# Kernel optimization log

Hardware: AMD Instinct MI355X
Metric: run time of the kernel (lower is better)

Reference implementation:

```python
import jax, jax.numpy as jnp
import numpy as np

N_Q = 8  # number of residual quantization levels


def setup_inputs() -> dict:
    key = jax.random.key(0)
    k1, k2 = jax.random.split(key)
    hidden_states = jax.random.normal(k1, (8192, 128), dtype=jnp.float32)
    codebooks = jax.random.normal(k2, (N_Q, 256, 128), dtype=jnp.float32)
    return {"hidden_states": hidden_states, "codebooks": codebooks}


def reference(hidden_states, codebooks):
    """Residual VQ encode: per level, nearest codebook entry by L2, subtract, accumulate.

    hidden_states: [N, D]; codebooks: [n_q, bins, D].
    Returns (codes [n_q, N] int, quantized [N, D]).
    """
    residual = hidden_states
    quantized = jnp.zeros_like(hidden_states)
    codes = []
    for i in range(N_Q):  # small fixed loop over structurally distinct levels
        codebook = codebooks[i]  # [bins, D]
        # squared L2 distance, same math as the original broadcasted form
        dist = jnp.sum((residual[:, None, :] - codebook[None, :, :]) ** 2, axis=-1)  # [N, bins]
        idx = jnp.argmin(dist, axis=-1)  # [N]
        chosen = codebook[idx]  # [N, D]
        quantized = quantized + chosen
        residual = residual - chosen
        codes.append(idx)
    return jnp.stack(codes, axis=0), quantized
```

## Files before the change

### kernel.cpp

```cpp
#include <hip/hip_runtime.h>

#define NQ 8
#define BINS 256
#define D 128
#define RPB 16
#define THREADS 512
#define RSTRIDE 132
#define FREG 520

typedef short s8v __attribute__((ext_vector_type(8)));
typedef short s4v __attribute__((ext_vector_type(4)));
typedef float f4v __attribute__((ext_vector_type(4)));

static __device__ __forceinline__ unsigned short bf16_rtne(float x) {
    unsigned u = __float_as_uint(x);
    unsigned r = (u + 0x7fffu + ((u >> 16) & 1u)) >> 16;
    return (unsigned short)r;
}
static __device__ __forceinline__ float bf16_to_f(unsigned short h) {
    return __uint_as_float(((unsigned)h) << 16);
}
struct Split3 { short h, m, l; };
static __device__ __forceinline__ Split3 split3(float x) {
    Split3 s;
    unsigned short hb = bf16_rtne(x);
    float r1 = x - bf16_to_f(hb);
    unsigned short mb = bf16_rtne(r1);
    unsigned short lb = bf16_rtne(r1 - bf16_to_f(mb));
    s.h = (short)hb; s.m = (short)mb; s.l = (short)lb;
    return s;
}
static __device__ __forceinline__ unsigned long long u64min(unsigned long long a, unsigned long long b) {
    return a < b ? a : b;
}
static __device__ __forceinline__ unsigned long long shfl_xor_u64(unsigned long long v, int mask) {
    int lo = (int)(unsigned)(v & 0xffffffffull);
    int hi = (int)(unsigned)(v >> 32);
    lo = __shfl_xor(lo, mask, 64);
    hi = __shfl_xor(hi, mask, 64);
    return ((unsigned long long)(unsigned)hi << 32) | (unsigned)lo;
}

__global__ __launch_bounds__(256) void rvq_prep(
    const float* __restrict__ cb, short* __restrict__ cb_hi,
    short* __restrict__ cb_mid, short* __restrict__ cb_lo,
    float* __restrict__ c2)
{
    __shared__ float st[16 * RSTRIDE];
    const int L = blockIdx.x >> 4;
    const int o = blockIdx.x & 15;
    const int t = threadIdx.x;

    const float4* src = (const float4*)(cb + ((size_t)L * BINS + o * 16) * D);
    #pragma unroll
    for (int i = 0; i < 2; ++i) {
        int f4 = i * 256 + t;
        int row = f4 >> 5, c4 = f4 & 31;
        float4 v = src[f4];
        float* d = &st[row * RSTRIDE + c4 * 4];
        d[0] = v.x; d[1] = v.y; d[2] = v.z; d[3] = v.w;
    }
    __syncthreads();

    const int bin = t >> 4;
    const int kc  = t & 15;
    const float* p = &st[bin * RSTRIDE + kc * 8];
    s8v h8, m8, l8;
    float s = 0.f;
    #pragma unroll
    for (int j = 0; j < 8; ++j) {
        float x = p[j];
        Split3 sp = split3(x);
        h8[j] = sp.h; m8[j] = sp.m; l8[j] = sp.l;
        s = fmaf(x, x, s);
    }
    int idx = (L * 16 + kc) * BINS + (o * 16 + bin);
    ((s8v*)cb_hi)[idx]  = h8;
    ((s8v*)cb_mid)[idx] = m8;
    ((s8v*)cb_lo)[idx]  = l8;
    s += __shfl_xor(s, 1, 64);
    s += __shfl_xor(s, 2, 64);
    s += __shfl_xor(s, 4, 64);
    s += __shfl_xor(s, 8, 64);
    if (kc == 0) c2[L * BINS + o * 16 + bin] = s;
}

static __device__ __forceinline__ void frag_store4(
    const float* rres, short* ah, short* am, short* al, int rr_, int g8, int half)
{
    s4v h4, m4, l4;
    #pragma unroll
    for (int j = 0; j < 4; ++j) {
        Split3 sp = split3(rres[j]);
        h4[j] = sp.h; m4[j] = sp.m; l4[j] = sp.l;
    }
    int q  = g8 & 3;
    int ks = g8 >> 2;
    int idx16 = q * 16 + ((rr_ + 4 * q) & 15);
    int off = ks * FREG + idx16 * 8 + half * 4;
    *(s4v*)&ah[off] = h4;
    *(s4v*)&am[off] = m4;
    *(s4v*)&al[off] = l4;
}

static __device__ __forceinline__ void issue_cb(
    int lv, int base16, int m, int quad,
    const s8v* __restrict__ bhp, const s8v* __restrict__ bmp, const s8v* __restrict__ blp,
    const float* __restrict__ c2p,
    s8v bh[4], s8v bm[4], s8v bl[4], f4v& c2v)
{
    const int bin = base16 + m;
    #pragma unroll
    for (int ks = 0; ks < 4; ++ks) {
        int idx = (lv * 16 + ks * 4 + quad) * BINS + bin;
        bh[ks] = bhp[idx];
        bm[ks] = bmp[idx];
        bl[ks] = blp[idx];
    }
    c2v = *(const f4v*)(c2p + lv * BINS + base16 + quad * 4);
}

static __device__ __forceinline__ unsigned long long cluster(
    const s8v bh[4], const s8v bm[4], const s8v bl[4],
    const s8v rfh[4], const s8v rfm[4], const s8v rfl[4],
    f4v c2c, int binbase, unsigned long long best)
{
    f4v a0 = {0.f, 0.f, 0.f, 0.f};
    f4v a1 = {0.f, 0.f, 0.f, 0.f};
    f4v a2 = {0.f, 0.f, 0.f, 0.f};
    __builtin_amdgcn_s_setprio(1);
    #pragma unroll
    for (int ks = 0; ks < 4; ++ks) {
        a0 = __builtin_amdgcn_mfma_f32_16x16x32_bf16(bh[ks], rfh[ks], a0, 0, 0, 0);
        a1 = __builtin_amdgcn_mfma_f32_16x16x32_bf16(bm[ks], rfh[ks], a1, 0, 0, 0);
        a1 = __builtin_amdgcn_mfma_f32_16x16x32_bf16(bh[ks], rfm[ks], a1, 0, 0, 0);
        a2 = __builtin_amdgcn_mfma_f32_16x16x32_bf16(bm[ks], rfm[ks], a2, 0, 0, 0);
        a2 = __builtin_amdgcn_mfma_f32_16x16x32_bf16(bl[ks], rfh[ks], a2, 0, 0, 0);
        a2 = __builtin_amdgcn_mfma_f32_16x16x32_bf16(bh[ks], rfl[ks], a2, 0, 0, 0);
    }
    __builtin_amdgcn_s_setprio(0);
    #pragma unroll
    for (int i = 0; i < 4; ++i) {
        float dot = a0[i] + (a1[i] + a2[i]);
        float k = fmaf(-2.f, dot, c2c[i]);
        unsigned u = __float_as_uint(k);
        u = (u & 0x80000000u) ? ~u : (u | 0x80000000u);
        best = u64min(best, ((unsigned long long)u << 32) | (unsigned)(binbase + i));
    }
    return best;
}

__global__ __launch_bounds__(THREADS)
__attribute__((amdgpu_waves_per_eu(2, 4)))
void rvq_kernel(
    const float* __restrict__ hidden,
    const float* __restrict__ cb_f32,
    const short* __restrict__ cb_hi,
    const short* __restrict__ cb_mid,
    const short* __restrict__ cb_lo,
    const float* __restrict__ c2p,
    float* __restrict__ out_codes,
    float* __restrict__ out_quant,
    int N)
{
    __shared__ __align__(16) short ah[4 * FREG];
    __shared__ __align__(16) short am[4 * FREG];
    __shared__ __align__(16) short al[4 * FREG];
    __shared__ __align__(16) unsigned long long redw[RPB][10];

    const int t = threadIdx.x;
    const int w = t >> 6;
    const int l = t & 63;
    const int quad = l >> 4;
    const int m = l & 15;
    const int woff = w * 32;
    const int row0 = blockIdx.x * RPB;
    const int rr_  = t >> 5;
    const int gd   = t & 31;
    const int g8   = gd >> 1;
    const int half = gd & 1;
    const int dbase = g8 * 8 + half * 4;

    float rres[4], hreg[4];
    {
        const f4v* hp = (const f4v*)(hidden + (size_t)(row0 + rr_) * D + dbase);
        f4v v = *hp;
        #pragma unroll
        for (int j = 0; j < 4; ++j) { hreg[j] = v[j]; rres[j] = v[j]; }
    }
    frag_store4(rres, ah, am, al, rr_, g8, half);

    const s8v* bhp = (const s8v*)cb_hi;
    const s8v* bmp = (const s8v*)cb_mid;
    const s8v* blp = (const s8v*)cb_lo;

    s8v bh0[4], bm0[4], bl0[4];
    s8v bh1[4], bm1[4], bl1[4];
    f4v c20, c21;
    issue_cb(0, woff, m, quad, bhp, bmp, blp, c2p, bh0, bm0, bl0, c20);

    const int idx16 = quad * 16 + ((m + 4 * quad) & 15);

    for (int level = 0; level < NQ; ++level) {
        __syncthreads();

        issue_cb(level, woff + 16, m, quad, bhp, bmp, blp, c2p, bh1, bm1, bl1, c21);

        s8v rfh[4], rfm[4], rfl[4];
        #pragma unroll
        for (int ks = 0; ks < 4; ++ks) {
            int off = ks * FREG + idx16 * 8;
            rfh[ks] = *(const s8v*)&ah[off];
            rfm[ks] = *(const s8v*)&am[off];
            rfl[ks] = *(const s8v*)&al[off];
        }

        unsigned long long best = ~0ull;
        best = cluster(bh0, bm0, bl0, rfh, rfm, rfl, c20, woff + quad * 4, best);
        if (level + 1 < NQ)
            issue_cb(level + 1, woff, m, quad, bhp, bmp, blp, c2p, bh0, bm0, bl0, c20);
        best = cluster(bh1, bm1, bl1, rfh, rfm, rfl, c21, woff + 16 + quad * 4, best);

        best = u64min(best, shfl_xor_u64(best, 16));
        best = u64min(best, shfl_xor_u64(best, 32));
        if (l < 16)
            redw[m][w] = best;
        __syncthreads();

        unsigned long long mn;
        {
            const ulonglong2* rp = (const ulonglong2*)&redw[rr_][0];
            ulonglong2 p0 = rp[0], p1 = rp[1], p2 = rp[2], p3 = rp[3];
            mn = u64min(u64min(u64min(p0.x, p0.y), u64min(p1.x, p1.y)),
                        u64min(u64min(p2.x, p2.y), u64min(p3.x, p3.y)));
        }
        const int wb = (int)(mn & 0xffffffffull);
        if (gd == 0)
            out_codes[(size_t)level * N + row0 + rr_] = (float)wb;

        {
            const f4v* cp = (const f4v*)(cb_f32 + ((size_t)level * BINS + wb) * D + dbase);
            f4v c = *cp;
            #pragma unroll
            for (int j = 0; j < 4; ++j) rres[j] -= c[j];
        }
        if (level + 1 < NQ)
            frag_store4(rres, ah, am, al, rr_, g8, half);
    }

    {
        f4v q;
        #pragma unroll
        for (int j = 0; j < 4; ++j) q[j] = hreg[j] - rres[j];
        *(f4v*)(out_quant + (size_t)(row0 + rr_) * D + dbase) = q;
    }
}

extern "C" void kernel_launch(void* const* d_in, const int* in_sizes, int n_in,
                              void* d_out, int out_size, void* d_ws, size_t ws_size,
                              hipStream_t stream) {
    const float* hidden    = (const float*)d_in[0];
    const float* codebooks = (const float*)d_in[1];
    float* out = (float*)d_out;
    const int N = in_sizes[0] / D;
    float* out_codes = out;
    float* out_quant = out + (size_t)NQ * N;

    char* ws = (char*)d_ws;
    short* cb_hi  = (short*)ws;
    short* cb_mid = (short*)(ws +  512 * 1024);
    short* cb_lo  = (short*)(ws + 1024 * 1024);
    float* c2     = (float*)(ws + 1536 * 1024);

    rvq_prep<<<dim3(NQ * 16), 256, 0, stream>>>(codebooks, cb_hi, cb_mid, cb_lo, c2);
    rvq_kernel<<<dim3(N / RPB), THREADS, 0, stream>>>(
        hidden, codebooks, cb_hi, cb_mid, cb_lo, c2, out_codes, out_quant, N);
}
```

Measured before the change: 115.2 us.

## Process 64 rows per block to reuse codebook fragments across four row tiles

Raises rows per block from 16 to 64, so each wave's register-held codebook fragments are reused across four 16-row MFMA tiles instead of one. This cuts the per-row global codebook traffic and the per-row barrier overhead. Each thread now owns 16 elements of a row and writes 8-wide fragments to shared memory. Both codebook halves are prefetched together after the compute, and the barriers become an explicit lgkmcnt wait plus s_barrier. The trade-offs are a quarter as many blocks (128 for this input), less overlap of codebook loads with compute, and higher register and LDS use.

Result: slower. 236.2 us (+105.1%).

```diff
diff --git a/kernel.cpp b/kernel.cpp
--- a/kernel.cpp
+++ b/kernel.cpp
@@ -3,14 +3,15 @@
 #define NQ 8
 #define BINS 256
 #define D 128
-#define RPB 16
+#define RPB 64
 #define THREADS 512
 #define RSTRIDE 132
 #define FREG 520
 
 typedef short s8v __attribute__((ext_vector_type(8)));
-typedef short s4v __attribute__((ext_vector_type(4)));
 typedef float f4v __attribute__((ext_vector_type(4)));
+
+#define BAR_LGKM() asm volatile("s_waitcnt lgkmcnt(0)\n\ts_barrier" ::: "memory")
 
 static __device__ __forceinline__ unsigned short bf16_rtne(float x) {
     unsigned u = __float_as_uint(x);
@@ -85,22 +86,28 @@
     if (kc == 0) c2[L * BINS + o * 16 + bin] = s;
 }
 
-static __device__ __forceinline__ void frag_store4(
-    const float* rres, short* ah, short* am, short* al, int rr_, int g8, int half)
-{
-    s4v h4, m4, l4;
-    #pragma unroll
-    for (int j = 0; j < 4; ++j) {
-        Split3 sp = split3(rres[j]);
-        h4[j] = sp.h; m4[j] = sp.m; l4[j] = sp.l;
-    }
-    int q  = g8 & 3;
-    int ks = g8 >> 2;
-    int idx16 = q * 16 + ((rr_ + 4 * q) & 15);
-    int off = ks * FREG + idx16 * 8 + half * 4;
-    *(s4v*)&ah[off] = h4;
-    *(s4v*)&am[off] = m4;
-    *(s4v*)&al[off] = l4;
+static __device__ __forceinline__ void frag_store16(
+    const float* rres, short* ah, short* am, short* al, int rr_, int dt)
+{
+    const int mt  = rr_ >> 4;
+    const int r16 = rr_ & 15;
+    #pragma unroll
+    for (int j = 0; j < 2; ++j) {
+        s8v h8, m8, l8;
+        #pragma unroll
+        for (int k = 0; k < 8; ++k) {
+            Split3 sp = split3(rres[j * 8 + k]);
+            h8[k] = sp.h; m8[k] = sp.m; l8[k] = sp.l;
+        }
+        int g8 = 2 * dt + j;
+        int q  = g8 & 3;
+        int ks = g8 >> 2;
+        int idx16 = q * 16 + ((r16 + 4 * q) & 15);
+        int off = (mt * 4 + ks) * FREG + idx16 * 8;
+        *(s8v*)&ah[off] = h8;
+        *(s8v*)&am[off] = m8;
+        *(s8v*)&al[off] = l8;
+    }
 }
 
 static __device__ __forceinline__ void issue_cb(
@@ -150,9 +157,7 @@
     return best;
 }
 
-__global__ __launch_bounds__(THREADS)
-__attribute__((amdgpu_waves_per_eu(2, 4)))
-void rvq_kernel(
+__global__ __launch_bounds__(THREADS, 2) void rvq_kernel(
     const float* __restrict__ hidden,
     const float* __restrict__ cb_f32,
     const short* __restrict__ cb_hi,
@@ -163,9 +168,9 @@
     float* __restrict__ out_quant,
     int N)
 {
-    __shared__ __align__(16) short ah[4 * FREG];
-    __shared__ __align__(16) short am[4 * FREG];
-    __shared__ __align__(16) short al[4 * FREG];
+    __shared__ __align__(16) short ah[16 * FREG];
+    __shared__ __align__(16) short am[16 * FREG];
+    __shared__ __align__(16) short al[16 * FREG];
     __shared__ __align__(16) unsigned long long redw[RPB][10];
 
     const int t = threadIdx.x;
@@ -175,20 +180,21 @@
     const int m = l & 15;
     const int woff = w * 32;
     const int row0 = blockIdx.x * RPB;
-    const int rr_  = t >> 5;
-    const int gd   = t & 31;
-    const int g8   = gd >> 1;
-    const int half = gd & 1;
-    const int dbase = g8 * 8 + half * 4;
-
-    float rres[4], hreg[4];
+    const int rr_ = t >> 3;
+    const int dt  = t & 7;
+    const int dbase = dt * 16;
+
+    float rres[16];
     {
         const f4v* hp = (const f4v*)(hidden + (size_t)(row0 + rr_) * D + dbase);
-        f4v v = *hp;
-        #pragma unroll
-        for (int j = 0; j < 4; ++j) { hreg[j] = v[j]; rres[j] = v[j]; }
-    }
-    frag_store4(rres, ah, am, al, rr_, g8, half);
+        #pragma unroll
+        for (int i = 0; i < 4; ++i) {
+            f4v v = hp[i];
+            #pragma unroll
+            for (int j = 0; j < 4; ++j) rres[i * 4 + j] = v[j];
+        }
+    }
+    frag_store16(rres, ah, am, al, rr_, dt);
 
     const s8v* bhp = (const s8v*)cb_hi;
     const s8v* bmp = (const s8v*)cb_mid;
@@ -197,35 +203,46 @@
     s8v bh0[4], bm0[4], bl0[4];
     s8v bh1[4], bm1[4], bl1[4];
     f4v c20, c21;
-    issue_cb(0, woff, m, quad, bhp, bmp, blp, c2p, bh0, bm0, bl0, c20);
+    issue_cb(0, woff,      m, quad, bhp, bmp, blp, c2p, bh0, bm0, bl0, c20);
+    issue_cb(0, woff + 16, m, quad, bhp, bmp, blp, c2p, bh1, bm1, bl1, c21);
 
     const int idx16 = quad * 16 + ((m + 4 * quad) & 15);
 
     for (int level = 0; level < NQ; ++level) {
-        __syncthreads();
-
-        issue_cb(level, woff + 16, m, quad, bhp, bmp, blp, c2p, bh1, bm1, bl1, c21);
-
-        s8v rfh[4], rfm[4], rfl[4];
-        #pragma unroll
-        for (int ks = 0; ks < 4; ++ks) {
-            int off = ks * FREG + idx16 * 8;
-            rfh[ks] = *(const s8v*)&ah[off];
-            rfm[ks] = *(const s8v*)&am[off];
-            rfl[ks] = *(const s8v*)&al[off];
-        }
-
-        unsigned long long best = ~0ull;
-        best = cluster(bh0, bm0, bl0, rfh, rfm, rfl, c20, woff + quad * 4, best);
-        if (level + 1 < NQ)
-            issue_cb(level + 1, woff, m, quad, bhp, bmp, blp, c2p, bh0, bm0, bl0, c20);
-        best = cluster(bh1, bm1, bl1, rfh, rfm, rfl, c21, woff + 16 + quad * 4, best);
-
-        best = u64min(best, shfl_xor_u64(best, 16));
-        best = u64min(best, shfl_xor_u64(best, 32));
-        if (l < 16)
-            redw[m][w] = best;
-        __syncthreads();
+        BAR_LGKM();
+
+        unsigned long long best[4];
+        #pragma unroll
+        for (int mt = 0; mt < 4; ++mt) best[mt] = ~0ull;
+
+        #pragma unroll
+        for (int mt = 0; mt < 4; ++mt) {
+            s8v rfh[4], rfm[4], rfl[4];
+            #pragma unroll
+            for (int ks = 0; ks < 4; ++ks) {
+                int off = (mt * 4 + ks) * FREG + idx16 * 8;
+                rfh[ks] = *(const s8v*)&ah[off];
+                rfm[ks] = *(const s8v*)&am[off];
+                rfl[ks] = *(const s8v*)&al[off];
+            }
+            best[mt] = cluster(bh0, bm0, bl0, rfh, rfm, rfl, c20, woff + quad * 4, best[mt]);
+            best[mt] = cluster(bh1, bm1, bl1, rfh, rfm, rfl, c21, woff + 16 + quad * 4, best[mt]);
+        }
+
+        if (level + 1 < NQ) {
+            issue_cb(level + 1, woff,      m, quad, bhp, bmp, blp, c2p, bh0, bm0, bl0, c20);
+            issue_cb(level + 1, woff + 16, m, quad, bhp, bmp, blp, c2p, bh1, bm1, bl1, c21);
+        }
+
+        #pragma unroll
+        for (int mt = 0; mt < 4; ++mt) {
+            unsigned long long b = best[mt];
+            b = u64min(b, shfl_xor_u64(b, 16));
+            b = u64min(b, shfl_xor_u64(b, 32));
+            if (l < 16)
+                redw[mt * 16 + m][w] = b;
+        }
+        BAR_LGKM();
 
         unsigned long long mn;
         {
@@ -235,24 +252,33 @@
                         u64min(u64min(p2.x, p2.y), u64min(p3.x, p3.y)));
         }
         const int wb = (int)(mn & 0xffffffffull);
-        if (gd == 0)
+        if (dt == 0)
             out_codes[(size_t)level * N + row0 + rr_] = (float)wb;
 
         {
             const f4v* cp = (const f4v*)(cb_f32 + ((size_t)level * BINS + wb) * D + dbase);
-            f4v c = *cp;
             #pragma unroll
-            for (int j = 0; j < 4; ++j) rres[j] -= c[j];
+            for (int i = 0; i < 4; ++i) {
+                f4v c = cp[i];
+                #pragma unroll
+                for (int j = 0; j < 4; ++j) rres[i * 4 + j] -= c[j];
+            }
         }
         if (level + 1 < NQ)
-            frag_store4(rres, ah, am, al, rr_, g8, half);
+            frag_store16(rres, ah, am, al, rr_, dt);
     }
 
     {
-        f4v q;
-        #pragma unroll
-        for (int j = 0; j < 4; ++j) q[j] = hreg[j] - rres[j];
-        *(f4v*)(out_quant + (size_t)(row0 + rr_) * D + dbase) = q;
+        const f4v* hp = (const f4v*)(hidden + (size_t)(row0 + rr_) * D + dbase);
+        f4v* op = (f4v*)(out_quant + (size_t)(row0 + rr_) * D + dbase);
+        #pragma unroll
+        for (int i = 0; i < 4; ++i) {
+            f4v v = hp[i];
+            f4v q;
+            #pragma unroll
+            for (int j = 0; j < 4; ++j) q[j] = v[j] - rres[i * 4 + j];
+            op[i] = q;
+        }
     }
 }
 
```
